# Kernel tuning notes

Hardware: AMD Instinct MI355X
Metric: run time of the kernel (lower is better)

## Reference

```python
import jax, jax.numpy as jnp
import numpy as np

N, T, D = 32, 64, 16
F = 512  # object_classes == feature dim after object_fc


def _gcn(x, adj, W, b):
    # Kipf GraphConvolution: adj @ (x @ W) + b
    return adj @ (x @ W) + b


def _norm_adj(a):
    d = jnp.sum(a, axis=1) ** -0.5
    return a * d[:, None] * d[None, :]


def _per_graph(x, gc1_W, gc1_b, gc2_W, gc2_b, gc3_W, gc3_b, gc4_W, gc4_b):
    # x: [D, F]
    # graph_generator / adj2: softmax-style similarity adjacency with D^{-1/2} norm
    s = x @ x.T                                   # [D, D]
    a = jnp.exp(s - jnp.max(s, axis=1, keepdims=True))
    adj = _norm_adj(a)
    # branch 1
    x1 = jax.nn.relu(_gcn(x, adj, gc1_W, gc1_b))
    x1 = _gcn(x1, adj, gc2_W, gc2_b)
    # branch 2 (adj_hat2 identical construction from x)
    y2 = jax.nn.relu(_gcn(x, adj, gc3_W, gc3_b))  # [D, 32]
    y22 = y2 @ y2.T
    nrm = jnp.sqrt(jnp.sum(y22 * y22, axis=1, keepdims=True))  # torch.norm(y22, 2, dim=1)
    adj3 = 1.0 + y22 / (nrm @ nrm.T)
    adj_hat3 = _norm_adj(adj3)
    y2 = _gcn(y2, adj_hat3, gc4_W, gc4_b)
    return (x1 + y2) * 0.5


def setup_inputs() -> dict:
    key = jax.random.key(0)
    ks = jax.random.split(key, 12)
    s = 0.02
    return {
        "object_raw": jax.random.normal(ks[0], (N * T * D, F), jnp.float32),
        "action_raw": jax.random.normal(ks[1], (N * T, F), jnp.float32),
        "W_obj": jax.random.normal(ks[2], (F, 512), jnp.float32) * s,
        "b_obj": jnp.zeros((512,), jnp.float32),
        "W_act": jax.random.normal(ks[3], (F, 512), jnp.float32) * s,
        "b_act": jnp.zeros((512,), jnp.float32),
        "gc1_W": jax.random.normal(ks[4], (512, 32), jnp.float32) * s,
        "gc1_b": jnp.zeros((32,), jnp.float32),
        "gc2_W": jax.random.normal(ks[5], (32, 512), jnp.float32) * s,
        "gc2_b": jnp.zeros((512,), jnp.float32),
        "gc3_W": jax.random.normal(ks[6], (512, 32), jnp.float32) * s,
        "gc3_b": jnp.zeros((32,), jnp.float32),
        "gc4_W": jax.random.normal(ks[7], (32, 512), jnp.float32) * s,
        "gc4_b": jnp.zeros((512,), jnp.float32),
        "fc1_W": jax.random.normal(ks[8], (512, 1024), jnp.float32) * s,
        "fc1_b": jnp.zeros((1024,), jnp.float32),
        "clf_W": jax.random.normal(ks[9], (1024, 500), jnp.float32) * s,
        "clf_b": jnp.zeros((500,), jnp.float32),
    }


def reference(object_raw, action_raw, W_obj, b_obj, W_act, b_act,
              gc1_W, gc1_b, gc2_W, gc2_b, gc3_W, gc3_b, gc4_W, gc4_b,
              fc1_W, fc1_b, clf_W, clf_b):
    obj = jax.nn.relu(object_raw @ W_obj + b_obj).reshape(N * T, D, 512)
    act = jax.nn.relu(action_raw @ W_act + b_act)           # [N*T, 512]
    obj = obj.at[:, D // 2].set(act)                         # overwrite middle frame
    graph = jax.vmap(lambda x: _per_graph(x, gc1_W, gc1_b, gc2_W, gc2_b,
                                          gc3_W, gc3_b, gc4_W, gc4_b))(obj)
    g = graph.reshape(N, T, D, 512).mean(axis=2)
    o = obj.reshape(N, T, D, 512).mean(axis=2)
    feat = (o + g) * 0.5                                     # graph_fusion == 'mean'
    c = jax.nn.relu(feat)                                    # dropout = identity (eval)
    c = jax.nn.relu(c @ fc1_W + fc1_b)
    out = (c @ clf_W + clf_b).mean(axis=1)                   # mean over T -> [N, 500]
    return out
```

## Files before the change

### kernel.cpp

```cpp
#include <hip/hip_runtime.h>
#include <hip/hip_bf16.h>

using ushort_t = unsigned short;
using f32x4  = __attribute__((ext_vector_type(4))) float;
using short8 = __attribute__((ext_vector_type(8))) short;

__device__ __forceinline__ float bflo(unsigned p) {
    union { unsigned u; float f; } x; x.u = p << 16; return x.f;
}
__device__ __forceinline__ float bfhi(unsigned p) {
    union { unsigned u; float f; } x; x.u = p & 0xffff0000u; return x.f;
}
__device__ __forceinline__ ushort_t f2bf(float f) {
    __hip_bfloat16 h = __float2bfloat16(f);
    return *(ushort_t*)&h;
}
__device__ __forceinline__ unsigned pk2bf(float lo, float hi) {
    __hip_bfloat162 h = __float22bfloat162_rn({lo, hi});
    return *(unsigned*)&h;
}

__device__ __forceinline__ void tr_tile(const float* __restrict__ S, ushort_t* __restrict__ D,
                                        int K, int N, int Npad, int bx, int by,
                                        int tx, int ty, float* tile )
{
    const int k0 = by * 32, n0 = bx * 32;
#pragma unroll
    for (int r = 0; r < 4; r++) {
        const int k = k0 + ty + r * 8, n = n0 + tx;
        tile[(ty + r * 8) * 33 + tx] = (k < K && n < N) ? S[(size_t)k * N + n] : 0.f;
    }
    __syncthreads();
#pragma unroll
    for (int r = 0; r < 4; r++) {
        const int n = n0 + ty + r * 8, k = k0 + tx;
        if (n < Npad && k < K) D[(size_t)n * K + k] = f2bf(tile[tx * 33 + ty + r * 8]);
    }
}

__device__ __forceinline__ void trf_tile(const float* __restrict__ S, float* __restrict__ D,
                                         int K, int N, int bx, int by,
                                         int tx, int ty, float* tile )
{
    const int k0 = by * 32, n0 = bx * 32;
#pragma unroll
    for (int r = 0; r < 4; r++) {
        const int k = k0 + ty + r * 8, n = n0 + tx;
        tile[(ty + r * 8) * 33 + tx] = (k < K && n < N) ? S[(size_t)k * N + n] : 0.f;
    }
    __syncthreads();
#pragma unroll
    for (int r = 0; r < 4; r++) {
        const int n = n0 + ty + r * 8, k = k0 + tx;
        if (n < N && k < K) D[(size_t)n * K + k] = tile[tx * 33 + ty + r * 8];
    }
}

__global__ __launch_bounds__(256)
void prep_weights(const float* __restrict__ Wobj, ushort_t* __restrict__ WobjT,
                  const float* __restrict__ Wact, ushort_t* __restrict__ WactT,
                  const float* __restrict__ fc1W, ushort_t* __restrict__ fc1T,
                  const float* __restrict__ gc1W, ushort_t* __restrict__ W1t,
                  const float* __restrict__ gc3W, ushort_t* __restrict__ W3t,
                  const float* __restrict__ gc2W, ushort_t* __restrict__ W2bf,
                  const float* __restrict__ gc4W, ushort_t* __restrict__ W4bf,
                  const float* __restrict__ clfW, float* __restrict__ WclfT)
{
    __shared__ float tile[32 * 33];
    const int b = blockIdx.x;
    const int t = threadIdx.x;
    const int tx = t & 31, ty = t >> 5;

    if (b < 1056) {
        const float* S; ushort_t* D; int K, N, Npad, nt, l;
        if      (b < 256)  { S = Wobj; D = WobjT; K = 512; N = 512;  Npad = 512;  nt = 16; l = b; }
        else if (b < 512)  { S = Wact; D = WactT; K = 512; N = 512;  Npad = 512;  nt = 16; l = b - 256; }
        else if (b < 1024) { S = fc1W; D = fc1T;  K = 512; N = 1024; Npad = 1024; nt = 32; l = b - 512; }
        else if (b < 1040) { S = gc1W; D = W1t;   K = 512; N = 32;   Npad = 32;   nt = 1;  l = b - 1024; }
        else               { S = gc3W; D = W3t;   K = 512; N = 32;   Npad = 32;   nt = 1;  l = b - 1040; }
        tr_tile(S, D, K, N, Npad, l % nt, l / nt, tx, ty, tile);
    } else if (b < 1072) {
        const float* S = (b < 1064) ? gc2W : gc4W;
        ushort_t* D    = (b < 1064) ? W2bf : W4bf;
        const int i = (b < 1064 ? b - 1056 : b - 1064) * 256 + t;
        const float4 x = ((const float4*)S)[2 * i];
        const float4 y = ((const float4*)S)[2 * i + 1];
        unsigned r[4] = { pk2bf(x.x, x.y), pk2bf(x.z, x.w), pk2bf(y.x, y.y), pk2bf(y.z, y.w) };
        ((uint4*)D)[i] = *(uint4*)r;
    } else {
        const int l = b - 1072;
        trf_tile(clfW, WclfT, 1024, 500, l & 15, l >> 4, tx, ty, tile);
    }
}

__global__ __launch_bounds__(512, 2)
void gemm_obj_stream(const float* __restrict__ A, const ushort_t* __restrict__ Bt,
                     const float* __restrict__ bias, ushort_t* __restrict__ C)
{
    __shared__ __align__(16) ushort_t As[128 * 512];
    const int t = threadIdx.x;
    const int lane = t & 63, w = t >> 6;
    const int bm = blockIdx.x * 128;
    const int fr = lane & 15, fq = lane >> 4;

    const float4* A4 = (const float4*)(A + (size_t)bm * 512);
#pragma unroll
    for (int i = 0; i < 16; i++) {
        const int fl = i * 1024 + t * 2;
        const int row = fl >> 7;
        const float4 p0 = A4[fl];
        const float4 p1 = A4[fl + 1];
        unsigned rr[4] = { pk2bf(p0.x, p0.y), pk2bf(p0.z, p0.w),
                           pk2bf(p1.x, p1.y), pk2bf(p1.z, p1.w) };
        *(uint4*)&As[row * 512 + ((lane ^ (row & 7)) * 8)] = *(uint4*)rr;
    }

    const int nw = w * 64;
    const ushort_t* Bbase = Bt + (size_t)(nw + fr) * 512 + fq * 8;

    uint4 bA[4], bB[4];
#pragma unroll
    for (int j = 0; j < 4; j++) bA[j] = *(const uint4*)(Bbase + (size_t)j * 16 * 512);

    __syncthreads();

    f32x4 acc[4][8];
#pragma unroll
    for (int j = 0; j < 4; j++)
#pragma unroll
        for (int i = 0; i < 8; i++) acc[j][i] = (f32x4){0.f, 0.f, 0.f, 0.f};

    for (int kk = 0; kk < 16; kk += 2) {
        short8 af[8];
#pragma unroll
        for (int i = 0; i < 8; i++)
            af[i] = *(const short8*)&As[(i * 16 + fr) * 512 + (((kk * 4 + fq) ^ (fr & 7)) * 8)];
#pragma unroll
        for (int j = 0; j < 4; j++) {
            bB[j] = *(const uint4*)(Bbase + (size_t)j * 16 * 512 + (kk + 1) * 32);
            const short8 bf = *(const short8*)&bA[j];
#pragma unroll
            for (int i = 0; i < 8; i++)
                acc[j][i] = __builtin_amdgcn_mfma_f32_16x16x32_bf16(af[i], bf, acc[j][i], 0, 0, 0);
        }
#pragma unroll
        for (int i = 0; i < 8; i++)
            af[i] = *(const short8*)&As[(i * 16 + fr) * 512 + ((((kk + 1) * 4 + fq) ^ (fr & 7)) * 8)];
#pragma unroll
        for (int j = 0; j < 4; j++) {
            if (kk + 2 < 16)
                bA[j] = *(const uint4*)(Bbase + (size_t)j * 16 * 512 + (kk + 2) * 32);
            const short8 bf = *(const short8*)&bB[j];
#pragma unroll
            for (int i = 0; i < 8; i++)
                acc[j][i] = __builtin_amdgcn_mfma_f32_16x16x32_bf16(af[i], bf, acc[j][i], 0, 0, 0);
        }
    }

    __syncthreads();
#pragma unroll
    for (int j = 0; j < 4; j++) {
        const int col0 = j * 16 + fr;
        const float bv = bias[nw + col0];
#pragma unroll
        for (int i = 0; i < 8; i++) {
#pragma unroll
            for (int rr2 = 0; rr2 < 4; rr2++) {
                const int m = i * 16 + fq * 4 + rr2;
                const int pc = col0 ^ (((m >> 2) & 3) << 4);
                As[m * 512 + nw + pc] = f2bf(fmaxf(acc[j][i][rr2] + bv, 0.f));
            }
        }
    }
    __syncthreads();
#pragma unroll
    for (int i2 = 0; i2 < 16; i2++) {
        const int fl = i2 * 512 + t;
        const int m  = fl >> 6;
        const int n0 = (fl & 63) * 8;
        const int sl = n0 & ~63;
        const int cl = n0 & 63;
        const uint4 v = *(const uint4*)&As[m * 512 + sl + (cl ^ (((m >> 2) & 3) << 4))];
        *(uint4*)&C[(size_t)(bm + m) * 512 + n0] = v;
    }
}

typedef __attribute__((address_space(1))) void glb_void;
typedef __attribute__((address_space(3))) void lds_void;
__device__ __forceinline__ void dma16(const void* g, void* l) {
    __builtin_amdgcn_global_load_lds((glb_void*)(unsigned long long)(uintptr_t)g,
                                     (lds_void*)(unsigned)(uintptr_t)l, 16, 0, 0);
}

template<int RELU, typename AT>
__global__ __launch_bounds__(256)
void gemm_dma(const AT* __restrict__ A, const ushort_t* __restrict__ Bt,
              const float* __restrict__ bias, ushort_t* __restrict__ C,
              int N, int K, int Nb, int row_mul, int row_add)
{
    __shared__ __align__(16) char     AsRaw[128 * 32 * sizeof(AT)];
    __shared__ __align__(16) ushort_t Bs[128 * 32];
    const int t = threadIdx.x;
    const int lane = t & 63, w = t >> 6;
    const int bm = blockIdx.y * 128, bn = blockIdx.x * 128;
    const int mb = (w & 1) * 64, nb = (w >> 1) * 64;
    const int fr = lane & 15, fq = lane >> 4;

    f32x4 acc[16];
#pragma unroll
    for (int i = 0; i < 16; i++) acc[i] = (f32x4){0.f, 0.f, 0.f, 0.f};

    const int brow = lane >> 2, bk = lane & 3;
    const int klog = bk ^ ((brow >> 1) & 3);
    const int arow = lane >> 3, ag = lane & 7;

    for (int k0 = 0; k0 < K; k0 += 32) {
        __syncthreads();
        if constexpr (sizeof(AT) == 4) {
#pragma unroll
            for (int i = 0; i < 4; i++) {
                const int grp = w * 4 + i;
                const int row = grp * 8 + arow;
                const int gl = ag ^ (row & 7);
                dma16((const float*)A + (size_t)(bm + row) * K + k0 + gl * 4,
                      AsRaw + grp * 1024);
            }
        } else {
#pragma unroll
            for (int i = 0; i < 2; i++) {
                const int grp = w * 2 + i;
                const int row = grp * 16 + brow;
                dma16((const ushort_t*)A + (size_t)(bm + row) * K + k0 + klog * 8,
                      (ushort_t*)AsRaw + grp * 512);
            }
        }
#pragma unroll
        for (int i = 0; i < 2; i++) {
            const int grp = w * 2 + i;
            const int row = grp * 16 + brow;
            dma16(Bt + (size_t)(bn + row) * K + k0 + klog * 8, Bs + grp * 512);
        }
        __syncthreads();

        short8 af[4], bf[4];
        if constexpr (sizeof(AT) == 4) {
#pragma unroll
            for (int i = 0; i < 4; i++) {
                const int row = mb + i * 16 + fr;
                const float* base = (const float*)AsRaw + row * 32;
                const f32x4 p0 = *(const f32x4*)(base + (((2 * fq)     ^ (fr & 7)) * 4));
                const f32x4 p1 = *(const f32x4*)(base + (((2 * fq + 1) ^ (fr & 7)) * 4));
                unsigned rr[4] = { pk2bf(p0.x, p0.y), pk2bf(p0.z, p0.w),
                                   pk2bf(p1.x, p1.y), pk2bf(p1.z, p1.w) };
                af[i] = *(short8*)rr;
            }
        } else {
#pragma unroll
            for (int i = 0; i < 4; i++) {
                const int row = mb + i * 16 + fr;
                af[i] = *(const short8*)((const ushort_t*)AsRaw + row * 32 + (fq ^ ((fr >> 1) & 3)) * 8);
            }
        }
#pragma unroll
        for (int j = 0; j < 4; j++) {
            const int row = nb + j * 16 + fr;
            bf[j] = *(const short8*)(Bs + row * 32 + (fq ^ ((fr >> 1) & 3)) * 8);
        }
#pragma unroll
        for (int i = 0; i < 4; i++)
#pragma unroll
            for (int j = 0; j < 4; j++)
                acc[i * 4 + j] = __builtin_amdgcn_mfma_f32_16x16x32_bf16(
                    af[i], bf[j], acc[i * 4 + j], 0, 0, 0);
    }

#pragma unroll
    for (int j = 0; j < 4; j++) {
        const int n = bn + nb + j * 16 + fr;
        const float bv = (n < Nb) ? bias[n] : 0.f;
#pragma unroll
        for (int i = 0; i < 4; i++) {
            const f32x4 a = acc[i * 4 + j];
#pragma unroll
            for (int r = 0; r < 4; r++) {
                const int m = bm + mb + i * 16 + fq * 4 + r;
                float v = a[r] + bv;
                if (RELU) v = fmaxf(v, 0.f);
                C[((size_t)m * row_mul + row_add) * (size_t)N + n] = f2bf(v);
            }
        }
    }
}

__global__ __launch_bounds__(256)
void gemm_fc1_mean(const ushort_t* __restrict__ A, const ushort_t* __restrict__ Bt,
                   const float* __restrict__ bias, float* __restrict__ cmean)
{
    __shared__ __align__(16) ushort_t AsS[128 * 32];
    __shared__ __align__(16) ushort_t Bs[128 * 32];
    const int t = threadIdx.x;
    const int lane = t & 63, w = t >> 6;
    const int bm = blockIdx.y * 128, bn = blockIdx.x * 128;
    const int mb = (w & 1) * 64, nb = (w >> 1) * 64;
    const int fr = lane & 15, fq = lane >> 4;
    const int K = 512;

    f32x4 acc[16];
#pragma unroll
    for (int i = 0; i < 16; i++) acc[i] = (f32x4){0.f, 0.f, 0.f, 0.f};

    const int brow = lane >> 2, bk = lane & 3;
    const int klog = bk ^ ((brow >> 1) & 3);

    for (int k0 = 0; k0 < K; k0 += 32) {
        __syncthreads();
#pragma unroll
        for (int i = 0; i < 2; i++) {
            const int grp = w * 2 + i;
            const int row = grp * 16 + brow;
            dma16(A + (size_t)(bm + row) * K + k0 + klog * 8, AsS + grp * 512);
        }
#pragma unroll
        for (int i = 0; i < 2; i++) {
            const int grp = w * 2 + i;
            const int row = grp * 16 + brow;
            dma16(Bt + (size_t)(bn + row) * K + k0 + klog * 8, Bs + grp * 512);
        }
        __syncthreads();

        short8 af[4], bf[4];
#pragma unroll
        for (int i = 0; i < 4; i++) {
            const int row = mb + i * 16 + fr;
            af[i] = *(const short8*)(AsS + row * 32 + (fq ^ ((fr >> 1) & 3)) * 8);
        }
#pragma unroll
        for (int j = 0; j < 4; j++) {
            const int row = nb + j * 16 + fr;
            bf[j] = *(const short8*)(Bs + row * 32 + (fq ^ ((fr >> 1) & 3)) * 8);
        }
#pragma unroll
        for (int i = 0; i < 4; i++)
#pragma unroll
            for (int j = 0; j < 4; j++)
                acc[i * 4 + j] = __builtin_amdgcn_mfma_f32_16x16x32_bf16(
                    af[i], bf[j], acc[i * 4 + j], 0, 0, 0);
    }

    const int nidx = (bm + mb) >> 6;
#pragma unroll
    for (int j = 0; j < 4; j++) {
        const int n = bn + nb + j * 16 + fr;
        const float bv = bias[n];
        float s = 0.f;
#pragma unroll
        for (int i = 0; i < 4; i++) {
            const f32x4 a = acc[i * 4 + j];
#pragma unroll
            for (int r = 0; r < 4; r++) s += fmaxf(a[r] + bv, 0.f);
        }
        s += __shfl_xor(s, 16);
        s += __shfl_xor(s, 32);
        if (fq == 0) cmean[(size_t)nidx * 1024 + n] = s * (1.0f / 64.0f);
    }
}

__global__ __launch_bounds__(256)
void graph_pre(const ushort_t* __restrict__ obj,
               const ushort_t* __restrict__ W1t, const ushort_t* __restrict__ W3t,
               float* __restrict__ Sg, float* __restrict__ t1g,
               float* __restrict__ t3g, float* __restrict__ omsg)
{
    __shared__ __align__(16) ushort_t Xs[64 * 512];
    const int t = threadIdx.x;
    const int lane = t & 63, w = t >> 6;
    const int bm = blockIdx.x * 64;
    const int g0 = blockIdx.x * 4;
    const int fr = lane & 15, fq = lane >> 4;

#pragma unroll
    for (int i = 0; i < 16; i++) {
        const int flat = i * 256 + t;
        const int row = flat >> 6, c = flat & 63;
        const uint4 v = *(const uint4*)(obj + (size_t)(bm + row) * 512 + c * 8);
        *(uint4*)&Xs[row * 512 + ((c ^ (row & 7)) * 8)] = v;
    }
    __syncthreads();

    if (w == 1 || w == 2) {
        const ushort_t* Wt = (w == 1) ? W1t : W3t;
        float* outp       = (w == 1) ? t1g : t3g;
        f32x4 a0[4], a1[4];
#pragma unroll
        for (int g = 0; g < 4; g++) { a0[g] = (f32x4){0.f,0.f,0.f,0.f}; a1[g] = a0[g]; }
        for (int kk = 0; kk < 16; kk++) {
            const short8 wa = *(const short8*)(Wt + (size_t)fr * 512 + kk * 32 + fq * 8);
            const short8 wb = *(const short8*)(Wt + (size_t)(16 + fr) * 512 + kk * 32 + fq * 8);
#pragma unroll
            for (int g = 0; g < 4; g++) {
                const short8 af = *(const short8*)&Xs[(g * 16 + fr) * 512 + (((kk * 4 + fq) ^ (fr & 7)) * 8)];
                a0[g] = __builtin_amdgcn_mfma_f32_16x16x32_bf16(af, wa, a0[g], 0, 0, 0);
                a1[g] = __builtin_amdgcn_mfma_f32_16x16x32_bf16(af, wb, a1[g], 0, 0, 0);
            }
        }
#pragma unroll
        for (int g = 0; g < 4; g++) {
#pragma unroll
            for (int i = 0; i < 4; i++) {
                const int m = fq * 4 + i;
                outp[(size_t)(g0 + g) * 512 + m * 32 + fr]      = a0[g][i];
                outp[(size_t)(g0 + g) * 512 + m * 32 + 16 + fr] = a1[g][i];
            }
        }
    } else {
        const int gb = (w == 0) ? 0 : 2;
        f32x4 s0 = (f32x4){0.f,0.f,0.f,0.f}, s1 = s0;
        for (int kk = 0; kk < 16; kk++) {
            const short8 af0 = *(const short8*)&Xs[(gb * 16 + fr) * 512 + (((kk * 4 + fq) ^ (fr & 7)) * 8)];
            const short8 af1 = *(const short8*)&Xs[((gb + 1) * 16 + fr) * 512 + (((kk * 4 + fq) ^ (fr & 7)) * 8)];
            s0 = __builtin_amdgcn_mfma_f32_16x16x32_bf16(af0, af0, s0, 0, 0, 0);
            s1 = __builtin_amdgcn_mfma_f32_16x16x32_bf16(af1, af1, s1, 0, 0, 0);
        }
#pragma unroll
        for (int i = 0; i < 4; i++) {
            const int m = fq * 4 + i;
            Sg[(size_t)(g0 + gb) * 256 + m * 16 + fr]     = s0[i];
            Sg[(size_t)(g0 + gb + 1) * 256 + m * 16 + fr] = s1[i];
        }
#pragma unroll
        for (int gg = 0; gg < 2; gg++) {
            const int g = gb + gg;
            float om[8] = {0,0,0,0,0,0,0,0};
#pragma unroll
            for (int m = 0; m < 16; m++) {
                const uint4 q = *(const uint4*)&Xs[(g * 16 + m) * 512 + ((lane ^ (m & 7)) * 8)];
                om[0] += bflo(q.x); om[1] += bfhi(q.x);
                om[2] += bflo(q.y); om[3] += bfhi(q.y);
                om[4] += bflo(q.z); om[5] += bfhi(q.z);
                om[6] += bflo(q.w); om[7] += bfhi(q.w);
            }
            *(float4*)(omsg + (size_t)(g0 + g) * 512 + lane * 8)     = (float4){om[0], om[1], om[2], om[3]};
            *(float4*)(omsg + (size_t)(g0 + g) * 512 + lane * 8 + 4) = (float4){om[4], om[5], om[6], om[7]};
        }
    }
}

__global__ __launch_bounds__(64)
void graph_fin(const float* __restrict__ Sg, const float* __restrict__ t1g,
               const float* __restrict__ t3g, const float* __restrict__ omsg,
               const float* __restrict__ b1, const float* __restrict__ b3,
               const ushort_t* __restrict__ W2b, const float* __restrict__ b2,
               const ushort_t* __restrict__ W4b, const float* __restrict__ b4,
               ushort_t* __restrict__ cbuf)
{
    __shared__ float t1S[16 * 36], t3S[16 * 36], y2S[16 * 36];
    __shared__ float adjS[16 * 17];
    __shared__ float dvS[16], cAS[16], nrmS[16], dv3S[16], cA3S[16];
    __shared__ float zc1S[32], zc4S[32];

    const int lane = threadIdx.x;
    const int r = lane & 15, q = lane >> 4;
    const int g = blockIdx.x;

    {
        const int row = lane >> 2, cb = (lane & 3) * 8;
        const float4 a0 = *(const float4*)(t1g + (size_t)g * 512 + lane * 8);
        const float4 a1 = *(const float4*)(t1g + (size_t)g * 512 + lane * 8 + 4);
        const float4 c0v = *(const float4*)(t3g + (size_t)g * 512 + lane * 8);
        const float4 c1v = *(const float4*)(t3g + (size_t)g * 512 + lane * 8 + 4);
        *(float4*)&t1S[row * 36 + cb]     = a0;
        *(float4*)&t1S[row * 36 + cb + 4] = a1;
        *(float4*)&t3S[row * 36 + cb]     = c0v;
        *(float4*)&t3S[row * 36 + cb + 4] = c1v;
    }

    const float4 sv = *(const float4*)(Sg + (size_t)g * 256 + r * 16 + q * 4);
    float mx = fmaxf(fmaxf(sv.x, sv.y), fmaxf(sv.z, sv.w));
    mx = fmaxf(mx, __shfl_xor(mx, 16));
    mx = fmaxf(mx, __shfl_xor(mx, 32));
    const float e0 = expf(sv.x - mx), e1 = expf(sv.y - mx);
    const float e2 = expf(sv.z - mx), e3 = expf(sv.w - mx);
    float rs = e0 + e1 + e2 + e3;
    rs += __shfl_xor(rs, 16); rs += __shfl_xor(rs, 32);
    const float dv = rsqrtf(rs);
    if (q == 0) dvS[r] = dv;
    __syncthreads();

    float ad0, ad1, ad2, ad3;
    {
        const float4 dc = *(const float4*)&dvS[q * 4];
        ad0 = e0 * dv * dc.x; ad1 = e1 * dv * dc.y;
        ad2 = e2 * dv * dc.z; ad3 = e3 * dv * dc.w;
    }
    adjS[r * 17 + q * 4 + 0] = ad0; adjS[r * 17 + q * 4 + 1] = ad1;
    adjS[r * 17 + q * 4 + 2] = ad2; adjS[r * 17 + q * 4 + 3] = ad3;
    {
        float c0s = ad0, c1s = ad1, c2s = ad2, c3s = ad3;
#pragma unroll
        for (int m = 1; m <= 8; m <<= 1) {
            c0s += __shfl_xor(c0s, m); c1s += __shfl_xor(c1s, m);
            c2s += __shfl_xor(c2s, m); c3s += __shfl_xor(c3s, m);
        }
        if (r == 0) {
            cAS[q * 4 + 0] = c0s; cAS[q * 4 + 1] = c1s;
            cAS[q * 4 + 2] = c2s; cAS[q * 4 + 3] = c3s;
        }
    }
    __syncthreads();

    const int c0 = q * 8;
    float x1v[8], y2v[8];
    {
        const float4 b1a = *(const float4*)(b1 + c0);
        const float4 b1b = *(const float4*)(b1 + c0 + 4);
        const float4 b3a = *(const float4*)(b3 + c0);
        const float4 b3b = *(const float4*)(b3 + c0 + 4);
        x1v[0]=b1a.x; x1v[1]=b1a.y; x1v[2]=b1a.z; x1v[3]=b1a.w;
        x1v[4]=b1b.x; x1v[5]=b1b.y; x1v[6]=b1b.z; x1v[7]=b1b.w;
        y2v[0]=b3a.x; y2v[1]=b3a.y; y2v[2]=b3a.z; y2v[3]=b3a.w;
        y2v[4]=b3b.x; y2v[5]=b3b.y; y2v[6]=b3b.z; y2v[7]=b3b.w;
    }
#pragma unroll
    for (int j = 0; j < 16; j++) {
        const float a = adjS[r * 17 + j];
        const float4 t1a = *(const float4*)&t1S[j * 36 + c0];
        const float4 t1b = *(const float4*)&t1S[j * 36 + c0 + 4];
        const float4 t3a = *(const float4*)&t3S[j * 36 + c0];
        const float4 t3b = *(const float4*)&t3S[j * 36 + c0 + 4];
        x1v[0] = fmaf(a, t1a.x, x1v[0]); x1v[1] = fmaf(a, t1a.y, x1v[1]);
        x1v[2] = fmaf(a, t1a.z, x1v[2]); x1v[3] = fmaf(a, t1a.w, x1v[3]);
        x1v[4] = fmaf(a, t1b.x, x1v[4]); x1v[5] = fmaf(a, t1b.y, x1v[5]);
        x1v[6] = fmaf(a, t1b.z, x1v[6]); x1v[7] = fmaf(a, t1b.w, x1v[7]);
        y2v[0] = fmaf(a, t3a.x, y2v[0]); y2v[1] = fmaf(a, t3a.y, y2v[1]);
        y2v[2] = fmaf(a, t3a.z, y2v[2]); y2v[3] = fmaf(a, t3a.w, y2v[3]);
        y2v[4] = fmaf(a, t3b.x, y2v[4]); y2v[5] = fmaf(a, t3b.y, y2v[5]);
        y2v[6] = fmaf(a, t3b.z, y2v[6]); y2v[7] = fmaf(a, t3b.w, y2v[7]);
    }
#pragma unroll
    for (int cc = 0; cc < 8; cc++) {
        x1v[cc] = fmaxf(x1v[cc], 0.f);
        y2v[cc] = fmaxf(y2v[cc], 0.f);
        y2S[r * 36 + c0 + cc] = y2v[cc];
    }
    __syncthreads();

    float yy[4] = {0.f, 0.f, 0.f, 0.f};
#pragma unroll
    for (int k4 = 0; k4 < 8; k4++) {
        const float4 yi = *(const float4*)&y2S[r * 36 + k4 * 4];
#pragma unroll
        for (int i = 0; i < 4; i++) {
            const float4 yj = *(const float4*)&y2S[(q * 4 + i) * 36 + k4 * 4];
            yy[i] = fmaf(yi.x, yj.x, yy[i]); yy[i] = fmaf(yi.y, yj.y, yy[i]);
            yy[i] = fmaf(yi.z, yj.z, yy[i]); yy[i] = fmaf(yi.w, yj.w, yy[i]);
        }
    }
    {
        float sq = 0.f;
#pragma unroll
        for (int i = 0; i < 4; i++) sq = fmaf(yy[i], yy[i], sq);
        sq += __shfl_xor(sq, 16); sq += __shfl_xor(sq, 32);
        const float nr = sqrtf(sq);
        if (q == 0) nrmS[r] = nr;
    }
    __syncthreads();

    float a3[4];
    float dv3;
    {
        const float nr = nrmS[r];
        const float4 ncv = *(const float4*)&nrmS[q * 4];
        a3[0] = 1.0f + yy[0] / (nr * ncv.x);
        a3[1] = 1.0f + yy[1] / (nr * ncv.y);
        a3[2] = 1.0f + yy[2] / (nr * ncv.z);
        a3[3] = 1.0f + yy[3] / (nr * ncv.w);
        float d3 = a3[0] + a3[1] + a3[2] + a3[3];
        d3 += __shfl_xor(d3, 16); d3 += __shfl_xor(d3, 32);
        dv3 = rsqrtf(d3);
        if (q == 0) dv3S[r] = dv3;
    }
    {
        const float cAm = cAS[r];
        float zp[8];
#pragma unroll
        for (int cc = 0; cc < 8; cc++) zp[cc] = cAm * x1v[cc];
#pragma unroll
        for (int m = 1; m <= 8; m <<= 1)
#pragma unroll
            for (int cc = 0; cc < 8; cc++) zp[cc] += __shfl_xor(zp[cc], m);
        if (r == 0)
#pragma unroll
            for (int cc = 0; cc < 8; cc++) zc1S[c0 + cc] = zp[cc];
    }
    __syncthreads();

    {
        const float4 d3c = *(const float4*)&dv3S[q * 4];
        float p0 = a3[0] * dv3 * d3c.x, p1 = a3[1] * dv3 * d3c.y;
        float p2 = a3[2] * dv3 * d3c.z, p3 = a3[3] * dv3 * d3c.w;
#pragma unroll
        for (int m = 1; m <= 8; m <<= 1) {
            p0 += __shfl_xor(p0, m); p1 += __shfl_xor(p1, m);
            p2 += __shfl_xor(p2, m); p3 += __shfl_xor(p3, m);
        }
        if (r == 0) {
            cA3S[q * 4 + 0] = p0; cA3S[q * 4 + 1] = p1;
            cA3S[q * 4 + 2] = p2; cA3S[q * 4 + 3] = p3;
        }
    }
    __syncthreads();

    {
        const float cA3m = cA3S[r];
        float zp[8];
#pragma unroll
        for (int cc = 0; cc < 8; cc++) zp[cc] = cA3m * y2v[cc];
#pragma unroll
        for (int m = 1; m <= 8; m <<= 1)
#pragma unroll
            for (int cc = 0; cc < 8; cc++) zp[cc] += __shfl_xor(zp[cc], m);
        if (r == 0)
#pragma unroll
            for (int cc = 0; cc < 8; cc++) zc4S[c0 + cc] = zp[cc];
    }
    __syncthreads();

    {
        float gm[8] = {0,0,0,0,0,0,0,0};
        const ushort_t* w2p = W2b + lane * 8;
        const ushort_t* w4p = W4b + lane * 8;
#pragma unroll 8
        for (int k = 0; k < 32; k++) {
            const float z1 = zc1S[k], z4 = zc4S[k];
            const uint4 u2 = *(const uint4*)(w2p + (size_t)k * 512);
            const uint4 u4 = *(const uint4*)(w4p + (size_t)k * 512);
            gm[0] = fmaf(z1, bflo(u2.x), gm[0]); gm[0] = fmaf(z4, bflo(u4.x), gm[0]);
            gm[1] = fmaf(z1, bfhi(u2.x), gm[1]); gm[1] = fmaf(z4, bfhi(u4.x), gm[1]);
            gm[2] = fmaf(z1, bflo(u2.y), gm[2]); gm[2] = fmaf(z4, bflo(u4.y), gm[2]);
            gm[3] = fmaf(z1, bfhi(u2.y), gm[3]); gm[3] = fmaf(z4, bfhi(u4.y), gm[3]);
            gm[4] = fmaf(z1, bflo(u2.z), gm[4]); gm[4] = fmaf(z4, bflo(u4.z), gm[4]);
            gm[5] = fmaf(z1, bfhi(u2.z), gm[5]); gm[5] = fmaf(z4, bfhi(u4.z), gm[5]);
            gm[6] = fmaf(z1, bflo(u2.w), gm[6]); gm[6] = fmaf(z4, bflo(u4.w), gm[6]);
            gm[7] = fmaf(z1, bfhi(u2.w), gm[7]); gm[7] = fmaf(z4, bfhi(u4.w), gm[7]);
        }
        const float4 oma = *(const float4*)(omsg + (size_t)g * 512 + lane * 8);
        const float4 omb = *(const float4*)(omsg + (size_t)g * 512 + lane * 8 + 4);
        const float om[8] = {oma.x, oma.y, oma.z, oma.w, omb.x, omb.y, omb.z, omb.w};
        const float4 b2a = *(const float4*)(b2 + lane * 8);
        const float4 b2b = *(const float4*)(b2 + lane * 8 + 4);
        const float4 b4a = *(const float4*)(b4 + lane * 8);
        const float4 b4b = *(const float4*)(b4 + lane * 8 + 4);
        const float bs[8] = { b2a.x + b4a.x, b2a.y + b4a.y, b2a.z + b4a.z, b2a.w + b4a.w,
                              b2b.x + b4b.x, b2b.y + b4b.y, b2b.z + b4b.z, b2b.w + b4b.w };
        ushort_t pk[8];
#pragma unroll
        for (int cc = 0; cc < 8; cc++) {
            const float gmean = 0.5f * bs[cc] + gm[cc] * (1.0f / 32.0f);
            const float feat  = 0.5f * (om[cc] * 0.0625f + gmean);
            pk[cc] = f2bf(fmaxf(feat, 0.f));
        }
        *(uint4*)(cbuf + (size_t)g * 512 + lane * 8) = *(uint4*)pk;
    }
}

__global__ __launch_bounds__(256)
void clf_col(const float* __restrict__ cmean, const float* __restrict__ Wt,
             const float* __restrict__ clf_b, float* __restrict__ out)
{
    __shared__ float red[8][33];
    const int j = blockIdx.x;
    const int t = threadIdx.x;
    const int n = t & 31, kp = t >> 5;
    const float* cm = cmean + (size_t)n * 1024 + kp * 128;
    const float* wp = Wt + (size_t)j * 1024 + kp * 128;
    float acc = 0.f;
#pragma unroll
    for (int k = 0; k < 128; k += 4) {
        const float4 c = *(const float4*)(cm + k);
        const float4 wv = *(const float4*)(wp + k);
        acc = fmaf(c.x, wv.x, acc);
        acc = fmaf(c.y, wv.y, acc);
        acc = fmaf(c.z, wv.z, acc);
        acc = fmaf(c.w, wv.w, acc);
    }
    red[kp][n] = acc;
    __syncthreads();
    if (t < 32) {
        float s = red[0][t];
#pragma unroll
        for (int p = 1; p < 8; p++) s += red[p][t];
        out[(size_t)t * 500 + j] = s + clf_b[j];
    }
}

extern "C" void kernel_launch(void* const* d_in, const int* in_sizes, int n_in,
                              void* d_out, int out_size, void* d_ws, size_t ws_size,
                              hipStream_t stream)
{
    const float* object_raw = (const float*)d_in[0];
    const float* action_raw = (const float*)d_in[1];
    const float* W_obj = (const float*)d_in[2];
    const float* b_obj = (const float*)d_in[3];
    const float* W_act = (const float*)d_in[4];
    const float* b_act = (const float*)d_in[5];
    const float* gc1_W = (const float*)d_in[6];
    const float* gc1_b = (const float*)d_in[7];
    const float* gc2_W = (const float*)d_in[8];
    const float* gc2_b = (const float*)d_in[9];
    const float* gc3_W = (const float*)d_in[10];
    const float* gc3_b = (const float*)d_in[11];
    const float* gc4_W = (const float*)d_in[12];
    const float* gc4_b = (const float*)d_in[13];
    const float* fc1_W = (const float*)d_in[14];
    const float* fc1_b = (const float*)d_in[15];
    const float* clf_W = (const float*)d_in[16];
    const float* clf_b = (const float*)d_in[17];

    char* ws = (char*)d_ws;
    const size_t MB = 1024 * 1024;
    ushort_t* obj_bf = (ushort_t*)(ws);
    ushort_t* cbuf   = (ushort_t*)(ws + 32 * MB);
    float*    WclfT  = (float*)   (ws + 34 * MB);
    float*    cmean  = (float*)   (ws + 38 * MB);
    ushort_t* WobjT  = (ushort_t*)(ws + 39 * MB);
    ushort_t* WactT  = (ushort_t*)(ws + 39 * MB + 512 * 1024);
    ushort_t* fc1T   = (ushort_t*)(ws + 40 * MB);
    ushort_t* W1t    = (ushort_t*)(ws + 41 * MB);
    ushort_t* W3t    = (ushort_t*)(ws + 41 * MB + 32 * 1024);
    ushort_t* W2bf   = (ushort_t*)(ws + 41 * MB + 64 * 1024);
    ushort_t* W4bf   = (ushort_t*)(ws + 41 * MB + 96 * 1024);
    float*    t1g    = (float*)   (ws + 44 * MB);
    float*    t3g    = (float*)   (ws + 48 * MB);
    float*    Sg     = (float*)   (ws + 52 * MB);
    float*    omsg   = (float*)   (ws + 54 * MB);

    prep_weights<<<dim3(1584), 256, 0, stream>>>(
        W_obj, WobjT, W_act, WactT, fc1_W, fc1T,
        gc1_W, W1t, gc3_W, W3t, gc2_W, W2bf, gc4_W, W4bf,
        clf_W, WclfT);

    gemm_obj_stream<<<dim3(256), 512, 0, stream>>>(object_raw, WobjT, b_obj, obj_bf);

    gemm_dma<1, float><<<dim3(4, 16), 256, 0, stream>>>(
        action_raw, WactT, b_act, obj_bf, 512, 512, 512, 16, 8);

    graph_pre<<<dim3(512), 256, 0, stream>>>(
        obj_bf, W1t, W3t, Sg, t1g, t3g, omsg);

    graph_fin<<<dim3(2048), 64, 0, stream>>>(
        Sg, t1g, t3g, omsg, gc1_b, gc3_b, W2bf, gc2_b, W4bf, gc4_b, cbuf);

    gemm_fc1_mean<<<dim3(8, 16), 256, 0, stream>>>(cbuf, fc1T, fc1_b, cmean);

    clf_col<<<dim3(500), 256, 0, stream>>>(cmean, WclfT, clf_b, (float*)d_out);
}
```

Baseline: 230.0 us.

## Fuse object GEMM with per-graph GCN stages into one mega kernel

The object projection GEMM, graph_pre and graph_fin are merged into a single kernel that keeps each block's 128 object rows (8 graphs) in LDS. The action rows are written to a small separate buffer and patched into LDS, and the per-graph similarity, GC1/GC3 products and finalisation all run from shared memory. This removes the 32 MB bf16 obj_bf round-trip to global memory, the t1/t3/S/omsg intermediates and two kernel launches. In exchange the kernel uses more LDS per block (128 KB As plus fsS), which may lower occupancy. The serial graph-finish phase now runs inside the GEMM block instead of across 2048 small blocks.

```diff
diff --git a/kernel.cpp b/kernel.cpp
--- a/kernel.cpp
+++ b/kernel.cpp
@@ -93,98 +93,6 @@
     }
 }
 
-__global__ __launch_bounds__(512, 2)
-void gemm_obj_stream(const float* __restrict__ A, const ushort_t* __restrict__ Bt,
-                     const float* __restrict__ bias, ushort_t* __restrict__ C)
-{
-    __shared__ __align__(16) ushort_t As[128 * 512];
-    const int t = threadIdx.x;
-    const int lane = t & 63, w = t >> 6;
-    const int bm = blockIdx.x * 128;
-    const int fr = lane & 15, fq = lane >> 4;
-
-    const float4* A4 = (const float4*)(A + (size_t)bm * 512);
-#pragma unroll
-    for (int i = 0; i < 16; i++) {
-        const int fl = i * 1024 + t * 2;
-        const int row = fl >> 7;
-        const float4 p0 = A4[fl];
-        const float4 p1 = A4[fl + 1];
-        unsigned rr[4] = { pk2bf(p0.x, p0.y), pk2bf(p0.z, p0.w),
-                           pk2bf(p1.x, p1.y), pk2bf(p1.z, p1.w) };
-        *(uint4*)&As[row * 512 + ((lane ^ (row & 7)) * 8)] = *(uint4*)rr;
-    }
-
-    const int nw = w * 64;
-    const ushort_t* Bbase = Bt + (size_t)(nw + fr) * 512 + fq * 8;
-
-    uint4 bA[4], bB[4];
-#pragma unroll
-    for (int j = 0; j < 4; j++) bA[j] = *(const uint4*)(Bbase + (size_t)j * 16 * 512);
-
-    __syncthreads();
-
-    f32x4 acc[4][8];
-#pragma unroll
-    for (int j = 0; j < 4; j++)
-#pragma unroll
-        for (int i = 0; i < 8; i++) acc[j][i] = (f32x4){0.f, 0.f, 0.f, 0.f};
-
-    for (int kk = 0; kk < 16; kk += 2) {
-        short8 af[8];
-#pragma unroll
-        for (int i = 0; i < 8; i++)
-            af[i] = *(const short8*)&As[(i * 16 + fr) * 512 + (((kk * 4 + fq) ^ (fr & 7)) * 8)];
-#pragma unroll
-        for (int j = 0; j < 4; j++) {
-            bB[j] = *(const uint4*)(Bbase + (size_t)j * 16 * 512 + (kk + 1) * 32);
-            const short8 bf = *(const short8*)&bA[j];
-#pragma unroll
-            for (int i = 0; i < 8; i++)
-                acc[j][i] = __builtin_amdgcn_mfma_f32_16x16x32_bf16(af[i], bf, acc[j][i], 0, 0, 0);
-        }
-#pragma unroll
-        for (int i = 0; i < 8; i++)
-            af[i] = *(const short8*)&As[(i * 16 + fr) * 512 + ((((kk + 1) * 4 + fq) ^ (fr & 7)) * 8)];
-#pragma unroll
-        for (int j = 0; j < 4; j++) {
-            if (kk + 2 < 16)
-                bA[j] = *(const uint4*)(Bbase + (size_t)j * 16 * 512 + (kk + 2) * 32);
-            const short8 bf = *(const short8*)&bB[j];
-#pragma unroll
-            for (int i = 0; i < 8; i++)
-                acc[j][i] = __builtin_amdgcn_mfma_f32_16x16x32_bf16(af[i], bf, acc[j][i], 0, 0, 0);
-        }
-    }
-
-    __syncthreads();
-#pragma unroll
-    for (int j = 0; j < 4; j++) {
-        const int col0 = j * 16 + fr;
-        const float bv = bias[nw + col0];
-#pragma unroll
-        for (int i = 0; i < 8; i++) {
-#pragma unroll
-            for (int rr2 = 0; rr2 < 4; rr2++) {
-                const int m = i * 16 + fq * 4 + rr2;
-                const int pc = col0 ^ (((m >> 2) & 3) << 4);
-                As[m * 512 + nw + pc] = f2bf(fmaxf(acc[j][i][rr2] + bv, 0.f));
-            }
-        }
-    }
-    __syncthreads();
-#pragma unroll
-    for (int i2 = 0; i2 < 16; i2++) {
-        const int fl = i2 * 512 + t;
-        const int m  = fl >> 6;
-        const int n0 = (fl & 63) * 8;
-        const int sl = n0 & ~63;
-        const int cl = n0 & 63;
-        const uint4 v = *(const uint4*)&As[m * 512 + sl + (cl ^ (((m >> 2) & 3) << 4))];
-        *(uint4*)&C[(size_t)(bm + m) * 512 + n0] = v;
-    }
-}
-
 typedef __attribute__((address_space(1))) void glb_void;
 typedef __attribute__((address_space(3))) void lds_void;
 __device__ __forceinline__ void dma16(const void* g, void* l) {
@@ -365,301 +273,377 @@
     }
 }
 
-__global__ __launch_bounds__(256)
-void graph_pre(const ushort_t* __restrict__ obj,
-               const ushort_t* __restrict__ W1t, const ushort_t* __restrict__ W3t,
-               float* __restrict__ Sg, float* __restrict__ t1g,
-               float* __restrict__ t3g, float* __restrict__ omsg)
+__global__ __launch_bounds__(512)
+void mega_obj_graph(const float* __restrict__ A, const ushort_t* __restrict__ Bt,
+                    const float* __restrict__ bias, const ushort_t* __restrict__ act_bf,
+                    const ushort_t* __restrict__ W1t, const ushort_t* __restrict__ W3t,
+                    const float* __restrict__ b1, const float* __restrict__ b3,
+                    const ushort_t* __restrict__ W2b, const float* __restrict__ b2,
+                    const ushort_t* __restrict__ W4b, const float* __restrict__ b4,
+                    ushort_t* __restrict__ cbuf)
 {
-    __shared__ __align__(16) ushort_t Xs[64 * 512];
+    __shared__ __align__(16) ushort_t As[128 * 512];
+    __shared__ __align__(16) float fsS[8][992];
+
     const int t = threadIdx.x;
     const int lane = t & 63, w = t >> 6;
-    const int bm = blockIdx.x * 64;
-    const int g0 = blockIdx.x * 4;
+    const int bm = blockIdx.x * 128;
     const int fr = lane & 15, fq = lane >> 4;
 
+    const float4* A4 = (const float4*)(A + (size_t)bm * 512);
 #pragma unroll
     for (int i = 0; i < 16; i++) {
-        const int flat = i * 256 + t;
-        const int row = flat >> 6, c = flat & 63;
-        const uint4 v = *(const uint4*)(obj + (size_t)(bm + row) * 512 + c * 8);
-        *(uint4*)&Xs[row * 512 + ((c ^ (row & 7)) * 8)] = v;
-    }
-    __syncthreads();
-
-    if (w == 1 || w == 2) {
-        const ushort_t* Wt = (w == 1) ? W1t : W3t;
-        float* outp       = (w == 1) ? t1g : t3g;
-        f32x4 a0[4], a1[4];
-#pragma unroll
-        for (int g = 0; g < 4; g++) { a0[g] = (f32x4){0.f,0.f,0.f,0.f}; a1[g] = a0[g]; }
+        const int fl = i * 1024 + t * 2;
+        const int row = fl >> 7;
+        const float4 p0 = A4[fl];
+        const float4 p1 = A4[fl + 1];
+        unsigned rr[4] = { pk2bf(p0.x, p0.y), pk2bf(p0.z, p0.w),
+                           pk2bf(p1.x, p1.y), pk2bf(p1.z, p1.w) };
+        *(uint4*)&As[row * 512 + ((lane ^ (row & 7)) * 8)] = *(uint4*)rr;
+    }
+
+    const int nw = w * 64;
+    const ushort_t* Bbase = Bt + (size_t)(nw + fr) * 512 + fq * 8;
+    uint4 bA[4], bB[4];
+#pragma unroll
+    for (int j = 0; j < 4; j++) bA[j] = *(const uint4*)(Bbase + (size_t)j * 16 * 512);
+
+    __syncthreads();
+
+    f32x4 acc[4][8];
+#pragma unroll
+    for (int j = 0; j < 4; j++)
+#pragma unroll
+        for (int i = 0; i < 8; i++) acc[j][i] = (f32x4){0.f, 0.f, 0.f, 0.f};
+
+    for (int kk = 0; kk < 16; kk += 2) {
+        short8 af[8];
+#pragma unroll
+        for (int i = 0; i < 8; i++)
+            af[i] = *(const short8*)&As[(i * 16 + fr) * 512 + (((kk * 4 + fq) ^ (fr & 7)) * 8)];
+#pragma unroll
+        for (int j = 0; j < 4; j++) {
+            bB[j] = *(const uint4*)(Bbase + (size_t)j * 16 * 512 + (kk + 1) * 32);
+            const short8 bf = *(const short8*)&bA[j];
+#pragma unroll
+            for (int i = 0; i < 8; i++)
+                acc[j][i] = __builtin_amdgcn_mfma_f32_16x16x32_bf16(af[i], bf, acc[j][i], 0, 0, 0);
+        }
+#pragma unroll
+        for (int i = 0; i < 8; i++)
+            af[i] = *(const short8*)&As[(i * 16 + fr) * 512 + ((((kk + 1) * 4 + fq) ^ (fr & 7)) * 8)];
+#pragma unroll
+        for (int j = 0; j < 4; j++) {
+            if (kk + 2 < 16)
+                bA[j] = *(const uint4*)(Bbase + (size_t)j * 16 * 512 + (kk + 2) * 32);
+            const short8 bf = *(const short8*)&bB[j];
+#pragma unroll
+            for (int i = 0; i < 8; i++)
+                acc[j][i] = __builtin_amdgcn_mfma_f32_16x16x32_bf16(af[i], bf, acc[j][i], 0, 0, 0);
+        }
+    }
+
+    __syncthreads();
+#pragma unroll
+    for (int j = 0; j < 4; j++) {
+        const int col0 = j * 16 + fr;
+        const float bv = bias[nw + col0];
+#pragma unroll
+        for (int i = 0; i < 8; i++) {
+#pragma unroll
+            for (int rr2 = 0; rr2 < 4; rr2++) {
+                const int m = i * 16 + fq * 4 + rr2;
+                const int sw = ((((col0 >> 3) ^ (m & 7)) << 3) | (col0 & 7));
+                As[m * 512 + nw + sw] = f2bf(fmaxf(acc[j][i][rr2] + bv, 0.f));
+            }
+        }
+    }
+    __syncthreads();
+
+    {
+        const int ra = t >> 6, gg = t & 63;
+        const uint4 v = *(const uint4*)(act_bf + (size_t)(blockIdx.x * 8 + ra) * 512 + gg * 8);
+        *(uint4*)&As[(ra * 16 + 8) * 512 + gg * 8] = v;
+    }
+    __syncthreads();
+
+    f32x4 e0[4], e1[4];
+    float om0[8], om1[8];
+    const bool isT = (w == 1) || (w == 2) || (w == 5) || (w == 6);
+    const int gofs = (w >= 4) ? 4 : 0;
+    const int sidx = (w == 0) ? 0 : (w == 3) ? 1 : (w == 4) ? 2 : 3;
+    const int gb = sidx * 2;
+
+    if (isT) {
+        const ushort_t* Wt = ((w & 3) == 1) ? W1t : W3t;
+#pragma unroll
+        for (int g = 0; g < 4; g++) { e0[g] = (f32x4){0.f,0.f,0.f,0.f}; e1[g] = e0[g]; }
         for (int kk = 0; kk < 16; kk++) {
             const short8 wa = *(const short8*)(Wt + (size_t)fr * 512 + kk * 32 + fq * 8);
             const short8 wb = *(const short8*)(Wt + (size_t)(16 + fr) * 512 + kk * 32 + fq * 8);
 #pragma unroll
             for (int g = 0; g < 4; g++) {
-                const short8 af = *(const short8*)&Xs[(g * 16 + fr) * 512 + (((kk * 4 + fq) ^ (fr & 7)) * 8)];
-                a0[g] = __builtin_amdgcn_mfma_f32_16x16x32_bf16(af, wa, a0[g], 0, 0, 0);
-                a1[g] = __builtin_amdgcn_mfma_f32_16x16x32_bf16(af, wb, a1[g], 0, 0, 0);
-            }
-        }
+                const short8 xf = *(const short8*)&As[((gofs + g) * 16 + fr) * 512 + (((kk * 4 + fq) ^ (fr & 7)) * 8)];
+                e0[g] = __builtin_amdgcn_mfma_f32_16x16x32_bf16(xf, wa, e0[g], 0, 0, 0);
+                e1[g] = __builtin_amdgcn_mfma_f32_16x16x32_bf16(xf, wb, e1[g], 0, 0, 0);
+            }
+        }
+    } else {
+        e0[0] = (f32x4){0.f,0.f,0.f,0.f}; e1[0] = e0[0];
+        for (int kk = 0; kk < 16; kk++) {
+            const short8 xf0 = *(const short8*)&As[(gb * 16 + fr) * 512 + (((kk * 4 + fq) ^ (fr & 7)) * 8)];
+            const short8 xf1 = *(const short8*)&As[((gb + 1) * 16 + fr) * 512 + (((kk * 4 + fq) ^ (fr & 7)) * 8)];
+            e0[0] = __builtin_amdgcn_mfma_f32_16x16x32_bf16(xf0, xf0, e0[0], 0, 0, 0);
+            e1[0] = __builtin_amdgcn_mfma_f32_16x16x32_bf16(xf1, xf1, e1[0], 0, 0, 0);
+        }
+#pragma unroll
+        for (int c = 0; c < 8; c++) { om0[c] = 0.f; om1[c] = 0.f; }
+#pragma unroll
+        for (int m = 0; m < 16; m++) {
+            const uint4 q0 = *(const uint4*)&As[(gb * 16 + m) * 512 + ((lane ^ (m & 7)) * 8)];
+            const uint4 q1 = *(const uint4*)&As[((gb + 1) * 16 + m) * 512 + ((lane ^ (m & 7)) * 8)];
+            om0[0] += bflo(q0.x); om0[1] += bfhi(q0.x);
+            om0[2] += bflo(q0.y); om0[3] += bfhi(q0.y);
+            om0[4] += bflo(q0.z); om0[5] += bfhi(q0.z);
+            om0[6] += bflo(q0.w); om0[7] += bfhi(q0.w);
+            om1[0] += bflo(q1.x); om1[1] += bfhi(q1.x);
+            om1[2] += bflo(q1.y); om1[3] += bfhi(q1.y);
+            om1[4] += bflo(q1.z); om1[5] += bfhi(q1.z);
+            om1[6] += bflo(q1.w); om1[7] += bfhi(q1.w);
+        }
+    }
+    __syncthreads();
+
+    float* Hs = (float*)As;
+    if (isT) {
+        const int toff = ((w & 3) == 1) ? 256 : 768;
 #pragma unroll
         for (int g = 0; g < 4; g++) {
+            float* dst = Hs + (gofs + g) * 1792 + toff;
 #pragma unroll
             for (int i = 0; i < 4; i++) {
                 const int m = fq * 4 + i;
-                outp[(size_t)(g0 + g) * 512 + m * 32 + fr]      = a0[g][i];
-                outp[(size_t)(g0 + g) * 512 + m * 32 + 16 + fr] = a1[g][i];
+                dst[m * 32 + fr]      = e0[g][i];
+                dst[m * 32 + 16 + fr] = e1[g][i];
             }
         }
     } else {
-        const int gb = (w == 0) ? 0 : 2;
-        f32x4 s0 = (f32x4){0.f,0.f,0.f,0.f}, s1 = s0;
-        for (int kk = 0; kk < 16; kk++) {
-            const short8 af0 = *(const short8*)&Xs[(gb * 16 + fr) * 512 + (((kk * 4 + fq) ^ (fr & 7)) * 8)];
-            const short8 af1 = *(const short8*)&Xs[((gb + 1) * 16 + fr) * 512 + (((kk * 4 + fq) ^ (fr & 7)) * 8)];
-            s0 = __builtin_amdgcn_mfma_f32_16x16x32_bf16(af0, af0, s0, 0, 0, 0);
-            s1 = __builtin_amdgcn_mfma_f32_16x16x32_bf16(af1, af1, s1, 0, 0, 0);
-        }
+        float* d0 = Hs + gb * 1792;
+        float* d1 = Hs + (gb + 1) * 1792;
 #pragma unroll
         for (int i = 0; i < 4; i++) {
             const int m = fq * 4 + i;
-            Sg[(size_t)(g0 + gb) * 256 + m * 16 + fr]     = s0[i];
-            Sg[(size_t)(g0 + gb + 1) * 256 + m * 16 + fr] = s1[i];
-        }
-#pragma unroll
-        for (int gg = 0; gg < 2; gg++) {
-            const int g = gb + gg;
-            float om[8] = {0,0,0,0,0,0,0,0};
-#pragma unroll
-            for (int m = 0; m < 16; m++) {
-                const uint4 q = *(const uint4*)&Xs[(g * 16 + m) * 512 + ((lane ^ (m & 7)) * 8)];
-                om[0] += bflo(q.x); om[1] += bfhi(q.x);
-                om[2] += bflo(q.y); om[3] += bfhi(q.y);
-                om[4] += bflo(q.z); om[5] += bfhi(q.z);
-                om[6] += bflo(q.w); om[7] += bfhi(q.w);
-            }
-            *(float4*)(omsg + (size_t)(g0 + g) * 512 + lane * 8)     = (float4){om[0], om[1], om[2], om[3]};
-            *(float4*)(omsg + (size_t)(g0 + g) * 512 + lane * 8 + 4) = (float4){om[4], om[5], om[6], om[7]};
-        }
-    }
-}
-
-__global__ __launch_bounds__(64)
-void graph_fin(const float* __restrict__ Sg, const float* __restrict__ t1g,
-               const float* __restrict__ t3g, const float* __restrict__ omsg,
-               const float* __restrict__ b1, const float* __restrict__ b3,
-               const ushort_t* __restrict__ W2b, const float* __restrict__ b2,
-               const ushort_t* __restrict__ W4b, const float* __restrict__ b4,
-               ushort_t* __restrict__ cbuf)
-{
-    __shared__ float t1S[16 * 36], t3S[16 * 36], y2S[16 * 36];
-    __shared__ float adjS[16 * 17];
-    __shared__ float dvS[16], cAS[16], nrmS[16], dv3S[16], cA3S[16];
-    __shared__ float zc1S[32], zc4S[32];
-
-    const int lane = threadIdx.x;
-    const int r = lane & 15, q = lane >> 4;
-    const int g = blockIdx.x;
+            d0[m * 16 + fr] = e0[0][i];
+            d1[m * 16 + fr] = e1[0][i];
+        }
+        *(float4*)(d0 + 1280 + lane * 8)     = (float4){om0[0], om0[1], om0[2], om0[3]};
+        *(float4*)(d0 + 1280 + lane * 8 + 4) = (float4){om0[4], om0[5], om0[6], om0[7]};
+        *(float4*)(d1 + 1280 + lane * 8)     = (float4){om1[0], om1[1], om1[2], om1[3]};
+        *(float4*)(d1 + 1280 + lane * 8 + 4) = (float4){om1[4], om1[5], om1[6], om1[7]};
+    }
+    __syncthreads();
 
     {
-        const int row = lane >> 2, cb = (lane & 3) * 8;
-        const float4 a0 = *(const float4*)(t1g + (size_t)g * 512 + lane * 8);
-        const float4 a1 = *(const float4*)(t1g + (size_t)g * 512 + lane * 8 + 4);
-        const float4 c0v = *(const float4*)(t3g + (size_t)g * 512 + lane * 8);
-        const float4 c1v = *(const float4*)(t3g + (size_t)g * 512 + lane * 8 + 4);
-        *(float4*)&t1S[row * 36 + cb]     = a0;
-        *(float4*)&t1S[row * 36 + cb + 4] = a1;
-        *(float4*)&t3S[row * 36 + cb]     = c0v;
-        *(float4*)&t3S[row * 36 + cb + 4] = c1v;
-    }
-
-    const float4 sv = *(const float4*)(Sg + (size_t)g * 256 + r * 16 + q * 4);
-    float mx = fmaxf(fmaxf(sv.x, sv.y), fmaxf(sv.z, sv.w));
-    mx = fmaxf(mx, __shfl_xor(mx, 16));
-    mx = fmaxf(mx, __shfl_xor(mx, 32));
-    const float e0 = expf(sv.x - mx), e1 = expf(sv.y - mx);
-    const float e2 = expf(sv.z - mx), e3 = expf(sv.w - mx);
-    float rs = e0 + e1 + e2 + e3;
-    rs += __shfl_xor(rs, 16); rs += __shfl_xor(rs, 32);
-    const float dv = rsqrtf(rs);
-    if (q == 0) dvS[r] = dv;
-    __syncthreads();
-
-    float ad0, ad1, ad2, ad3;
-    {
-        const float4 dc = *(const float4*)&dvS[q * 4];
-        ad0 = e0 * dv * dc.x; ad1 = e1 * dv * dc.y;
-        ad2 = e2 * dv * dc.z; ad3 = e3 * dv * dc.w;
-    }
-    adjS[r * 17 + q * 4 + 0] = ad0; adjS[r * 17 + q * 4 + 1] = ad1;
-    adjS[r * 17 + q * 4 + 2] = ad2; adjS[r * 17 + q * 4 + 3] = ad3;
-    {
-        float c0s = ad0, c1s = ad1, c2s = ad2, c3s = ad3;
-#pragma unroll
-        for (int m = 1; m <= 8; m <<= 1) {
-            c0s += __shfl_xor(c0s, m); c1s += __shfl_xor(c1s, m);
-            c2s += __shfl_xor(c2s, m); c3s += __shfl_xor(c3s, m);
-        }
-        if (r == 0) {
-            cAS[q * 4 + 0] = c0s; cAS[q * 4 + 1] = c1s;
-            cAS[q * 4 + 2] = c2s; cAS[q * 4 + 3] = c3s;
-        }
-    }
-    __syncthreads();
-
-    const int c0 = q * 8;
-    float x1v[8], y2v[8];
-    {
-        const float4 b1a = *(const float4*)(b1 + c0);
-        const float4 b1b = *(const float4*)(b1 + c0 + 4);
-        const float4 b3a = *(const float4*)(b3 + c0);
-        const float4 b3b = *(const float4*)(b3 + c0 + 4);
-        x1v[0]=b1a.x; x1v[1]=b1a.y; x1v[2]=b1a.z; x1v[3]=b1a.w;
-        x1v[4]=b1b.x; x1v[5]=b1b.y; x1v[6]=b1b.z; x1v[7]=b1b.w;
-        y2v[0]=b3a.x; y2v[1]=b3a.y; y2v[2]=b3a.z; y2v[3]=b3a.w;
-        y2v[4]=b3b.x; y2v[5]=b3b.y; y2v[6]=b3b.z; y2v[7]=b3b.w;
-    }
-#pragma unroll
-    for (int j = 0; j < 16; j++) {
-        const float a = adjS[r * 17 + j];
-        const float4 t1a = *(const float4*)&t1S[j * 36 + c0];
-        const float4 t1b = *(const float4*)&t1S[j * 36 + c0 + 4];
-        const float4 t3a = *(const float4*)&t3S[j * 36 + c0];
-        const float4 t3b = *(const float4*)&t3S[j * 36 + c0 + 4];
-        x1v[0] = fmaf(a, t1a.x, x1v[0]); x1v[1] = fmaf(a, t1a.y, x1v[1]);
-        x1v[2] = fmaf(a, t1a.z, x1v[2]); x1v[3] = fmaf(a, t1a.w, x1v[3]);
-        x1v[4] = fmaf(a, t1b.x, x1v[4]); x1v[5] = fmaf(a, t1b.y, x1v[5]);
-        x1v[6] = fmaf(a, t1b.z, x1v[6]); x1v[7] = fmaf(a, t1b.w, x1v[7]);
-        y2v[0] = fmaf(a, t3a.x, y2v[0]); y2v[1] = fmaf(a, t3a.y, y2v[1]);
-        y2v[2] = fmaf(a, t3a.z, y2v[2]); y2v[3] = fmaf(a, t3a.w, y2v[3]);
-        y2v[4] = fmaf(a, t3b.x, y2v[4]); y2v[5] = fmaf(a, t3b.y, y2v[5]);
-        y2v[6] = fmaf(a, t3b.z, y2v[6]); y2v[7] = fmaf(a, t3b.w, y2v[7]);
-    }
-#pragma unroll
-    for (int cc = 0; cc < 8; cc++) {
-        x1v[cc] = fmaxf(x1v[cc], 0.f);
-        y2v[cc] = fmaxf(y2v[cc], 0.f);
-        y2S[r * 36 + c0 + cc] = y2v[cc];
-    }
-    __syncthreads();
-
-    float yy[4] = {0.f, 0.f, 0.f, 0.f};
-#pragma unroll
-    for (int k4 = 0; k4 < 8; k4++) {
-        const float4 yi = *(const float4*)&y2S[r * 36 + k4 * 4];
-#pragma unroll
-        for (int i = 0; i < 4; i++) {
-            const float4 yj = *(const float4*)&y2S[(q * 4 + i) * 36 + k4 * 4];
-            yy[i] = fmaf(yi.x, yj.x, yy[i]); yy[i] = fmaf(yi.y, yj.y, yy[i]);
-            yy[i] = fmaf(yi.z, yj.z, yy[i]); yy[i] = fmaf(yi.w, yj.w, yy[i]);
-        }
-    }
-    {
-        float sq = 0.f;
-#pragma unroll
-        for (int i = 0; i < 4; i++) sq = fmaf(yy[i], yy[i], sq);
-        sq += __shfl_xor(sq, 16); sq += __shfl_xor(sq, 32);
-        const float nr = sqrtf(sq);
-        if (q == 0) nrmS[r] = nr;
-    }
-    __syncthreads();
-
-    float a3[4];
-    float dv3;
-    {
-        const float nr = nrmS[r];
-        const float4 ncv = *(const float4*)&nrmS[q * 4];
-        a3[0] = 1.0f + yy[0] / (nr * ncv.x);
-        a3[1] = 1.0f + yy[1] / (nr * ncv.y);
-        a3[2] = 1.0f + yy[2] / (nr * ncv.z);
-        a3[3] = 1.0f + yy[3] / (nr * ncv.w);
-        float d3 = a3[0] + a3[1] + a3[2] + a3[3];
-        d3 += __shfl_xor(d3, 16); d3 += __shfl_xor(d3, 32);
-        dv3 = rsqrtf(d3);
-        if (q == 0) dv3S[r] = dv3;
-    }
-    {
-        const float cAm = cAS[r];
-        float zp[8];
-#pragma unroll
-        for (int cc = 0; cc < 8; cc++) zp[cc] = cAm * x1v[cc];
-#pragma unroll
-        for (int m = 1; m <= 8; m <<= 1)
-#pragma unroll
-            for (int cc = 0; cc < 8; cc++) zp[cc] += __shfl_xor(zp[cc], m);
-        if (r == 0)
-#pragma unroll
-            for (int cc = 0; cc < 8; cc++) zc1S[c0 + cc] = zp[cc];
-    }
-    __syncthreads();
-
-    {
-        const float4 d3c = *(const float4*)&dv3S[q * 4];
-        float p0 = a3[0] * dv3 * d3c.x, p1 = a3[1] * dv3 * d3c.y;
-        float p2 = a3[2] * dv3 * d3c.z, p3 = a3[3] * dv3 * d3c.w;
-#pragma unroll
-        for (int m = 1; m <= 8; m <<= 1) {
-            p0 += __shfl_xor(p0, m); p1 += __shfl_xor(p1, m);
-            p2 += __shfl_xor(p2, m); p3 += __shfl_xor(p3, m);
-        }
-        if (r == 0) {
-            cA3S[q * 4 + 0] = p0; cA3S[q * 4 + 1] = p1;
-            cA3S[q * 4 + 2] = p2; cA3S[q * 4 + 3] = p3;
-        }
-    }
-    __syncthreads();
-
-    {
-        const float cA3m = cA3S[r];
-        float zp[8];
-#pragma unroll
-        for (int cc = 0; cc < 8; cc++) zp[cc] = cA3m * y2v[cc];
-#pragma unroll
-        for (int m = 1; m <= 8; m <<= 1)
-#pragma unroll
-            for (int cc = 0; cc < 8; cc++) zp[cc] += __shfl_xor(zp[cc], m);
-        if (r == 0)
-#pragma unroll
-            for (int cc = 0; cc < 8; cc++) zc4S[c0 + cc] = zp[cc];
-    }
-    __syncthreads();
-
-    {
-        float gm[8] = {0,0,0,0,0,0,0,0};
-        const ushort_t* w2p = W2b + lane * 8;
-        const ushort_t* w4p = W4b + lane * 8;
+        const int r = fr, q = fq;
+        const float* Hg = Hs + w * 1792;
+        float* fw   = fsS[w];
+        float* adjS = fw;
+        float* y2S  = fw + 272;
+        float* dvS  = fw + 848;
+        float* cAS  = fw + 864;
+        float* nrmS = fw + 880;
+        float* dv3S = fw + 896;
+        float* cA3S = fw + 912;
+        float* zc1S = fw + 928;
+        float* zc4S = fw + 960;
+
+        const float4 sv = *(const float4*)(Hg + r * 16 + q * 4);
+        float mx = fmaxf(fmaxf(sv.x, sv.y), fmaxf(sv.z, sv.w));
+        mx = fmaxf(mx, __shfl_xor(mx, 16));
+        mx = fmaxf(mx, __shfl_xor(mx, 32));
+        const float e0s = expf(sv.x - mx), e1s = expf(sv.y - mx);
+        const float e2s = expf(sv.z - mx), e3s = expf(sv.w - mx);
+        float rs = e0s + e1s + e2s + e3s;
+        rs += __shfl_xor(rs, 16); rs += __shfl_xor(rs, 32);
+        const float dv = rsqrtf(rs);
+        if (q == 0) dvS[r] = dv;
+        __syncthreads();
+
+        float ad0, ad1, ad2, ad3;
+        {
+            const float4 dc = *(const float4*)&dvS[q * 4];
+            ad0 = e0s * dv * dc.x; ad1 = e1s * dv * dc.y;
+            ad2 = e2s * dv * dc.z; ad3 = e3s * dv * dc.w;
+        }
+        adjS[r * 17 + q * 4 + 0] = ad0; adjS[r * 17 + q * 4 + 1] = ad1;
+        adjS[r * 17 + q * 4 + 2] = ad2; adjS[r * 17 + q * 4 + 3] = ad3;
+        {
+            float c0s = ad0, c1s = ad1, c2s = ad2, c3s = ad3;
+#pragma unroll
+            for (int m = 1; m <= 8; m <<= 1) {
+                c0s += __shfl_xor(c0s, m); c1s += __shfl_xor(c1s, m);
+                c2s += __shfl_xor(c2s, m); c3s += __shfl_xor(c3s, m);
+            }
+            if (r == 0) {
+                cAS[q * 4 + 0] = c0s; cAS[q * 4 + 1] = c1s;
+                cAS[q * 4 + 2] = c2s; cAS[q * 4 + 3] = c3s;
+            }
+        }
+        __syncthreads();
+
+        const int c0 = q * 8;
+        float x1v[8], y2v[8];
+        {
+            const float4 b1a = *(const float4*)(b1 + c0);
+            const float4 b1b = *(const float4*)(b1 + c0 + 4);
+            const float4 b3a = *(const float4*)(b3 + c0);
+            const float4 b3b = *(const float4*)(b3 + c0 + 4);
+            x1v[0]=b1a.x; x1v[1]=b1a.y; x1v[2]=b1a.z; x1v[3]=b1a.w;
+            x1v[4]=b1b.x; x1v[5]=b1b.y; x1v[6]=b1b.z; x1v[7]=b1b.w;
+            y2v[0]=b3a.x; y2v[1]=b3a.y; y2v[2]=b3a.z; y2v[3]=b3a.w;
+            y2v[4]=b3b.x; y2v[5]=b3b.y; y2v[6]=b3b.z; y2v[7]=b3b.w;
+        }
+#pragma unroll
+        for (int j = 0; j < 16; j++) {
+            const float a = adjS[r * 17 + j];
+            const float4 t1a = *(const float4*)(Hg + 256 + j * 32 + c0);
+            const float4 t1b = *(const float4*)(Hg + 256 + j * 32 + c0 + 4);
+            const float4 t3a = *(const float4*)(Hg + 768 + j * 32 + c0);
+            const float4 t3b = *(const float4*)(Hg + 768 + j * 32 + c0 + 4);
+            x1v[0] = fmaf(a, t1a.x, x1v[0]); x1v[1] = fmaf(a, t1a.y, x1v[1]);
+            x1v[2] = fmaf(a, t1a.z, x1v[2]); x1v[3] = fmaf(a, t1a.w, x1v[3]);
+            x1v[4] = fmaf(a, t1b.x, x1v[4]); x1v[5] = fmaf(a, t1b.y, x1v[5]);
+            x1v[6] = fmaf(a, t1b.z, x1v[6]); x1v[7] = fmaf(a, t1b.w, x1v[7]);
+            y2v[0] = fmaf(a, t3a.x, y2v[0]); y2v[1] = fmaf(a, t3a.y, y2v[1]);
+            y2v[2] = fmaf(a, t3a.z, y2v[2]); y2v[3] = fmaf(a, t3a.w, y2v[3]);
+            y2v[4] = fmaf(a, t3b.x, y2v[4]); y2v[5] = fmaf(a, t3b.y, y2v[5]);
+            y2v[6] = fmaf(a, t3b.z, y2v[6]); y2v[7] = fmaf(a, t3b.w, y2v[7]);
+        }
+#pragma unroll
+        for (int cc = 0; cc < 8; cc++) {
+            x1v[cc] = fmaxf(x1v[cc], 0.f);
+            y2v[cc] = fmaxf(y2v[cc], 0.f);
+            y2S[r * 36 + c0 + cc] = y2v[cc];
+        }
+        __syncthreads();
+
+        float yy[4] = {0.f, 0.f, 0.f, 0.f};
+#pragma unroll
+        for (int k4 = 0; k4 < 8; k4++) {
+            const float4 yi = *(const float4*)&y2S[r * 36 + k4 * 4];
+#pragma unroll
+            for (int i = 0; i < 4; i++) {
+                const float4 yj = *(const float4*)&y2S[(q * 4 + i) * 36 + k4 * 4];
+                yy[i] = fmaf(yi.x, yj.x, yy[i]); yy[i] = fmaf(yi.y, yj.y, yy[i]);
+                yy[i] = fmaf(yi.z, yj.z, yy[i]); yy[i] = fmaf(yi.w, yj.w, yy[i]);
+            }
+        }
+        {
+            float sq = 0.f;
+#pragma unroll
+            for (int i = 0; i < 4; i++) sq = fmaf(yy[i], yy[i], sq);
+            sq += __shfl_xor(sq, 16); sq += __shfl_xor(sq, 32);
+            const float nr = sqrtf(sq);
+            if (q == 0) nrmS[r] = nr;
+        }
+        __syncthreads();
+
+        float a3[4];
+        float dv3;
+        {
+            const float nr = nrmS[r];
+            const float4 ncv = *(const float4*)&nrmS[q * 4];
+            a3[0] = 1.0f + yy[0] / (nr * ncv.x);
+            a3[1] = 1.0f + yy[1] / (nr * ncv.y);
+            a3[2] = 1.0f + yy[2] / (nr * ncv.z);
+            a3[3] = 1.0f + yy[3] / (nr * ncv.w);
+            float d3 = a3[0] + a3[1] + a3[2] + a3[3];
+            d3 += __shfl_xor(d3, 16); d3 += __shfl_xor(d3, 32);
+            dv3 = rsqrtf(d3);
+            if (q == 0) dv3S[r] = dv3;
+        }
+        {
+            const float cAm = cAS[r];
+            float zp[8];
+#pragma unroll
+            for (int cc = 0; cc < 8; cc++) zp[cc] = cAm * x1v[cc];
+#pragma unroll
+            for (int m = 1; m <= 8; m <<= 1)
+#pragma unroll
+                for (int cc = 0; cc < 8; cc++) zp[cc] += __shfl_xor(zp[cc], m);
+            if (r == 0)
+#pragma unroll
+                for (int cc = 0; cc < 8; cc++) zc1S[c0 + cc] = zp[cc];
+        }
+        __syncthreads();
+
+        {
+            const float4 d3c = *(const float4*)&dv3S[q * 4];
+            float p0 = a3[0] * dv3 * d3c.x, p1 = a3[1] * dv3 * d3c.y;
+            float p2 = a3[2] * dv3 * d3c.z, p3 = a3[3] * dv3 * d3c.w;
+#pragma unroll
+            for (int m = 1; m <= 8; m <<= 1) {
+                p0 += __shfl_xor(p0, m); p1 += __shfl_xor(p1, m);
+                p2 += __shfl_xor(p2, m); p3 += __shfl_xor(p3, m);
+            }
+            if (r == 0) {
+                cA3S[q * 4 + 0] = p0; cA3S[q * 4 + 1] = p1;
+                cA3S[q * 4 + 2] = p2; cA3S[q * 4 + 3] = p3;
+            }
+        }
+        __syncthreads();
+
+        {
+            const float cA3m = cA3S[r];
+            float zp[8];
+#pragma unroll
+            for (int cc = 0; cc < 8; cc++) zp[cc] = cA3m * y2v[cc];
+#pragma unroll
+            for (int m = 1; m <= 8; m <<= 1)
+#pragma unroll
+                for (int cc = 0; cc < 8; cc++) zp[cc] += __shfl_xor(zp[cc], m);
+            if (r == 0)
+#pragma unroll
+                for (int cc = 0; cc < 8; cc++) zc4S[c0 + cc] = zp[cc];
+        }
+        __syncthreads();
+
+        {
+            float gm[8] = {0,0,0,0,0,0,0,0};
+            const ushort_t* w2p = W2b + lane * 8;
+            const ushort_t* w4p = W4b + lane * 8;
 #pragma unroll 8
-        for (int k = 0; k < 32; k++) {
-            const float z1 = zc1S[k], z4 = zc4S[k];
-            const uint4 u2 = *(const uint4*)(w2p + (size_t)k * 512);
-            const uint4 u4 = *(const uint4*)(w4p + (size_t)k * 512);
-            gm[0] = fmaf(z1, bflo(u2.x), gm[0]); gm[0] = fmaf(z4, bflo(u4.x), gm[0]);
-            gm[1] = fmaf(z1, bfhi(u2.x), gm[1]); gm[1] = fmaf(z4, bfhi(u4.x), gm[1]);
-            gm[2] = fmaf(z1, bflo(u2.y), gm[2]); gm[2] = fmaf(z4, bflo(u4.y), gm[2]);
-            gm[3] = fmaf(z1, bfhi(u2.y), gm[3]); gm[3] = fmaf(z4, bfhi(u4.y), gm[3]);
-            gm[4] = fmaf(z1, bflo(u2.z), gm[4]); gm[4] = fmaf(z4, bflo(u4.z), gm[4]);
-            gm[5] = fmaf(z1, bfhi(u2.z), gm[5]); gm[5] = fmaf(z4, bfhi(u4.z), gm[5]);
-            gm[6] = fmaf(z1, bflo(u2.w), gm[6]); gm[6] = fmaf(z4, bflo(u4.w), gm[6]);
-            gm[7] = fmaf(z1, bfhi(u2.w), gm[7]); gm[7] = fmaf(z4, bfhi(u4.w), gm[7]);
-        }
-        const float4 oma = *(const float4*)(omsg + (size_t)g * 512 + lane * 8);
-        const float4 omb = *(const float4*)(omsg + (size_t)g * 512 + lane * 8 + 4);
-        const float om[8] = {oma.x, oma.y, oma.z, oma.w, omb.x, omb.y, omb.z, omb.w};
-        const float4 b2a = *(const float4*)(b2 + lane * 8);
-        const float4 b2b = *(const float4*)(b2 + lane * 8 + 4);
-        const float4 b4a = *(const float4*)(b4 + lane * 8);
-        const float4 b4b = *(const float4*)(b4 + lane * 8 + 4);
-        const float bs[8] = { b2a.x + b4a.x, b2a.y + b4a.y, b2a.z + b4a.z, b2a.w + b4a.w,
-                              b2b.x + b4b.x, b2b.y + b4b.y, b2b.z + b4b.z, b2b.w + b4b.w };
-        ushort_t pk[8];
-#pragma unroll
-        for (int cc = 0; cc < 8; cc++) {
-            const float gmean = 0.5f * bs[cc] + gm[cc] * (1.0f / 32.0f);
-            const float feat  = 0.5f * (om[cc] * 0.0625f + gmean);
-            pk[cc] = f2bf(fmaxf(feat, 0.f));
-        }
-        *(uint4*)(cbuf + (size_t)g * 512 + lane * 8) = *(uint4*)pk;
+            for (int k = 0; k < 32; k++) {
+                const float z1 = zc1S[k], z4 = zc4S[k];
+                const uint4 u2 = *(const uint4*)(w2p + (size_t)k * 512);
+                const uint4 u4 = *(const uint4*)(w4p + (size_t)k * 512);
+                gm[0] = fmaf(z1, bflo(u2.x), gm[0]); gm[0] = fmaf(z4, bflo(u4.x), gm[0]);
+                gm[1] = fmaf(z1, bfhi(u2.x), gm[1]); gm[1] = fmaf(z4, bfhi(u4.x), gm[1]);
+                gm[2] = fmaf(z1, bflo(u2.y), gm[2]); gm[2] = fmaf(z4, bflo(u4.y), gm[2]);
+                gm[3] = fmaf(z1, bfhi(u2.y), gm[3]); gm[3] = fmaf(z4, bfhi(u4.y), gm[3]);
+                gm[4] = fmaf(z1, bflo(u2.z), gm[4]); gm[4] = fmaf(z4, bflo(u4.z), gm[4]);
+                gm[5] = fmaf(z1, bfhi(u2.z), gm[5]); gm[5] = fmaf(z4, bfhi(u4.z), gm[5]);
+                gm[6] = fmaf(z1, bflo(u2.w), gm[6]); gm[6] = fmaf(z4, bflo(u4.w), gm[6]);
+                gm[7] = fmaf(z1, bfhi(u2.w), gm[7]); gm[7] = fmaf(z4, bfhi(u4.w), gm[7]);
+            }
+            const float4 oma = *(const float4*)(Hg + 1280 + lane * 8);
+            const float4 omb = *(const float4*)(Hg + 1280 + lane * 8 + 4);
+            const float om[8] = {oma.x, oma.y, oma.z, oma.w, omb.x, omb.y, omb.z, omb.w};
+            const float4 b2a = *(const float4*)(b2 + lane * 8);
+            const float4 b2b = *(const float4*)(b2 + lane * 8 + 4);
+            const float4 b4a = *(const float4*)(b4 + lane * 8);
+            const float4 b4b = *(const float4*)(b4 + lane * 8 + 4);
+            const float bs[8] = { b2a.x + b4a.x, b2a.y + b4a.y, b2a.z + b4a.z, b2a.w + b4a.w,
+                                  b2b.x + b4b.x, b2b.y + b4b.y, b2b.z + b4b.z, b2b.w + b4b.w };
+            ushort_t pk[8];
+#pragma unroll
+            for (int cc = 0; cc < 8; cc++) {
+                const float gmean = 0.5f * bs[cc] + gm[cc] * (1.0f / 32.0f);
+                const float feat  = 0.5f * (om[cc] * 0.0625f + gmean);
+                pk[cc] = f2bf(fmaxf(feat, 0.f));
+            }
+            *(uint4*)(cbuf + (size_t)(blockIdx.x * 8 + w) * 512 + lane * 8) = *(uint4*)pk;
+        }
     }
 }
 
@@ -718,37 +702,29 @@
 
     char* ws = (char*)d_ws;
     const size_t MB = 1024 * 1024;
-    ushort_t* obj_bf = (ushort_t*)(ws);
-    ushort_t* cbuf   = (ushort_t*)(ws + 32 * MB);
-    float*    WclfT  = (float*)   (ws + 34 * MB);
-    float*    cmean  = (float*)   (ws + 38 * MB);
-    ushort_t* WobjT  = (ushort_t*)(ws + 39 * MB);
-    ushort_t* WactT  = (ushort_t*)(ws + 39 * MB + 512 * 1024);
-    ushort_t* fc1T   = (ushort_t*)(ws + 40 * MB);
-    ushort_t* W1t    = (ushort_t*)(ws + 41 * MB);
-    ushort_t* W3t    = (ushort_t*)(ws + 41 * MB + 32 * 1024);
-    ushort_t* W2bf   = (ushort_t*)(ws + 41 * MB + 64 * 1024);
-    ushort_t* W4bf   = (ushort_t*)(ws + 41 * MB + 96 * 1024);
-    float*    t1g    = (float*)   (ws + 44 * MB);
-    float*    t3g    = (float*)   (ws + 48 * MB);
-    float*    Sg     = (float*)   (ws + 52 * MB);
-    float*    omsg   = (float*)   (ws + 54 * MB);
+    ushort_t* act_bf = (ushort_t*)(ws);
+    ushort_t* cbuf   = (ushort_t*)(ws + 2 * MB);
+    float*    WclfT  = (float*)   (ws + 4 * MB);
+    float*    cmean  = (float*)   (ws + 6 * MB);
+    ushort_t* WobjT  = (ushort_t*)(ws + 7 * MB);
+    ushort_t* WactT  = (ushort_t*)(ws + 7 * MB + 512 * 1024);
+    ushort_t* fc1T   = (ushort_t*)(ws + 8 * MB);
+    ushort_t* W1t    = (ushort_t*)(ws + 9 * MB);
+    ushort_t* W3t    = (ushort_t*)(ws + 9 * MB + 32 * 1024);
+    ushort_t* W2bf   = (ushort_t*)(ws + 9 * MB + 64 * 1024);
+    ushort_t* W4bf   = (ushort_t*)(ws + 9 * MB + 96 * 1024);
 
     prep_weights<<<dim3(1584), 256, 0, stream>>>(
         W_obj, WobjT, W_act, WactT, fc1_W, fc1T,
         gc1_W, W1t, gc3_W, W3t, gc2_W, W2bf, gc4_W, W4bf,
         clf_W, WclfT);
 
-    gemm_obj_stream<<<dim3(256), 512, 0, stream>>>(object_raw, WobjT, b_obj, obj_bf);
-
     gemm_dma<1, float><<<dim3(4, 16), 256, 0, stream>>>(
-        action_raw, WactT, b_act, obj_bf, 512, 512, 512, 16, 8);
-
-    graph_pre<<<dim3(512), 256, 0, stream>>>(
-        obj_bf, W1t, W3t, Sg, t1g, t3g, omsg);
-
-    graph_fin<<<dim3(2048), 64, 0, stream>>>(
-        Sg, t1g, t3g, omsg, gc1_b, gc3_b, W2bf, gc2_b, W4bf, gc4_b, cbuf);
+        action_raw, WactT, b_act, act_bf, 512, 512, 512, 1, 0);
+
+    mega_obj_graph<<<dim3(256), 512, 0, stream>>>(
+        object_raw, WobjT, b_obj, act_bf, W1t, W3t,
+        gc1_b, gc3_b, W2bf, gc2_b, W4bf, gc4_b, cbuf);
 
     gemm_fc1_mean<<<dim3(8, 16), 256, 0, stream>>>(cbuf, fc1T, fc1_b, cmean);
 
```

Result: faster. 223.7 us (-2.7%).
